# Kernel optimization log

Hardware: AMD Instinct MI355X
Metric: run time of the kernel (lower is better)

## Reference

```python
import jax, jax.numpy as jnp
import numpy as np

B, S, D, H = 2, 2048, 1024, 16
HD = D // H  # 64
MASK_VAL = -10000.0


def setup_inputs() -> dict:
    key = jax.random.key(0)
    ks = jax.random.split(key, 8)
    sc = 0.02
    q_features = jax.random.normal(ks[0], (B, S, D), jnp.float32)
    kv_features = jax.random.normal(ks[1], (B, S, D), jnp.float32)
    # causal mask, broadcastable (1,1,S,S)
    mask = jnp.tril(jnp.ones((S, S), jnp.bool_))[None, None]
    Wq = jax.random.normal(ks[2], (D, D), jnp.float32) * sc
    bq = jnp.zeros((D,), jnp.float32)
    Wkv = jax.random.normal(ks[3], (D, 2 * D), jnp.float32) * sc
    bkv = jnp.zeros((2 * D,), jnp.float32)
    Wp = jax.random.normal(ks[4], (D, D), jnp.float32) * sc
    bp = jnp.zeros((D,), jnp.float32)
    return {"q_features": q_features, "kv_features": kv_features, "mask": mask,
            "Wq": Wq, "bq": bq, "Wkv": Wkv, "bkv": bkv, "Wp": Wp, "bp": bp}


def _split_heads(t):
    # (B,S,D) -> (B,H,S,HD)
    return t.reshape(B, S, H, HD).transpose(0, 2, 1, 3)


def reference(q_features, kv_features, mask, Wq, bq, Wkv, bkv, Wp, bp):
    query = q_features @ Wq + bq            # (B,S,D)
    kv = kv_features @ Wkv + bkv            # (B,S,2D)
    key, value = jnp.split(kv, 2, axis=-1)
    q = _split_heads(query)                 # (B,H,S,HD)
    k = _split_heads(key)
    v = _split_heads(value)
    scores = jnp.einsum('bhqd,bhkd->bhqk', q, k) / jnp.sqrt(jnp.float32(HD))
    scores = jnp.where(mask, scores, jnp.asarray(MASK_VAL, scores.dtype))
    attn = jax.nn.softmax(scores, axis=-1)  # (B,H,S,S)
    out = jnp.einsum('bhqk,bhkd->bhqd', attn, v)
    out = out.transpose(0, 2, 1, 3).reshape(B, S, D)  # merge heads
    return out @ Wp + bp
```

## Files before the change

### kernel.cpp

```cpp
#include <hip/hip_runtime.h>

typedef unsigned short u16;
typedef unsigned int u32;
typedef __attribute__((ext_vector_type(4))) unsigned short us4;
typedef __attribute__((ext_vector_type(8))) unsigned short us8;
typedef __attribute__((ext_vector_type(4))) short s16x4;
typedef __attribute__((ext_vector_type(8))) __bf16 bf16x8;
typedef __attribute__((ext_vector_type(4))) float floatx4;

#define S_ 2048
#define D_ 1024
#define QSC 0.18033688f

__device__ __forceinline__ float b2f(u16 u) {
  unsigned v = ((unsigned)u) << 16;
  return __builtin_bit_cast(float, v);
}
__device__ __forceinline__ u16 f2bf(float f) {
  unsigned u = __builtin_bit_cast(unsigned, f);
  unsigned r = (u + 0x7fffu + ((u >> 16) & 1u)) >> 16;
  return (u16)r;
}
__device__ __forceinline__ u16 f2bf_rhu(float f) {
  return (u16)((__builtin_bit_cast(unsigned, f) + 0x8000u) >> 16);
}

typedef const __attribute__((address_space(1))) u32* gas_t;
typedef __attribute__((address_space(3))) u32* las_t;
__device__ __forceinline__ void gload16(const u16* g, u16* l) {
  __builtin_amdgcn_global_load_lds((gas_t)g, (las_t)l, 16, 0, 0);
}

#define PBAR()                                   \
  {                                              \
    __builtin_amdgcn_sched_barrier(0);           \
    asm volatile("" ::: "memory");               \
    __builtin_amdgcn_s_barrier();                \
    asm volatile("" ::: "memory");               \
    __builtin_amdgcn_sched_barrier(0);           \
  }
#define WAITVM(N) asm volatile("s_waitcnt vmcnt(" #N ")" ::: "memory")

__global__ __launch_bounds__(256) void prep(
    const float* __restrict__ qf, const float* __restrict__ kvf,
    const float* __restrict__ Wq, const float* __restrict__ Wkv,
    const float* __restrict__ Wp, u16* __restrict__ qa, u16* __restrict__ kva,
    u16* __restrict__ Wqt, u16* __restrict__ Wkvt, u16* __restrict__ Wpt) {
  int bid = blockIdx.x, tid = threadIdx.x;
  if (bid < 4096) {
    const float* src = (bid < 2048) ? qf : kvf;
    u16* dst = (bid < 2048) ? qa : kva;
    size_t i = ((size_t)(bid & 2047) * 256 + tid) * 8;
    floatx4 a = *(const floatx4*)(src + i);
    floatx4 b = *(const floatx4*)(src + i + 4);
    us8 r;
#pragma unroll
    for (int j = 0; j < 4; j++) { r[j] = f2bf(a[j]); r[4 + j] = f2bf(b[j]); }
    *(us8*)(dst + i) = r;
  } else {
    int t = bid - 4096;
    const float* src; u16* dst; int R, C;
    if (t < 1024)      { src = Wq;  dst = Wqt;  R = 1024; C = 1024; }
    else if (t < 3072) { t -= 1024; src = Wkv; dst = Wkvt; R = 1024; C = 2048; }
    else               { t -= 3072; src = Wp;  dst = Wpt;  R = 1024; C = 1024; }
    int bx = t % (C >> 5), by = t / (C >> 5);
    __shared__ u16 tile[32][33];
    int tx = tid & 31, ty = tid >> 5;
    int x = bx * 32 + tx;
    for (int i = ty; i < 32; i += 8)
      tile[i][tx] = f2bf(src[(size_t)(by * 32 + i) * C + x]);
    __syncthreads();
    int r = tid >> 3, c4 = tid & 7;
    us4 v;
#pragma unroll
    for (int j = 0; j < 4; j++) v[j] = tile[c4 * 4 + j][r];
    *(us4*)&dst[(size_t)(bx * 32 + r) * R + by * 32 + c4 * 4] = v;
  }
}

template <int MODE>
__device__ __forceinline__ void gemm256(
    const u16* __restrict__ A, const u16* __restrict__ Bt,
    const float* __restrict__ bias, void* __restrict__ C0,
    u16* __restrict__ C1, int N, int m0, int n0, u16* smem, float cscale) {
  int tid = threadIdx.x;
  int w = tid >> 6, lane = tid & 63;
  int quad = lane >> 4, l16 = lane & 15;
  int wr = w >> 2, wc = w & 3;

  int srow = w * 32 + (lane >> 2);
  int gchunk = ((lane & 3) ^ ((lane >> 3) & 3)) << 3;
  const u16* Asrc = A + (size_t)(m0 + srow) * 1024 + gchunk;
  const u16* Bsrc = Bt + (size_t)(n0 + srow) * 1024 + gchunk;
  u16* Adst = smem + w * 1024;
  u16* Bdst = smem + 32768 + w * 1024;

  int swz = (quad ^ ((l16 >> 1) & 3)) << 3;
  int aoff = (wr * 128 + l16) * 32 + swz;
  int boff = 32768 + (wc * 64 + l16) * 32 + swz;

  floatx4 acc[8][4] = {};

#define STG(t)                                                 \
  {                                                            \
    int s_ = (t) & 3;                                          \
    gload16(Asrc + (t) * 32, Adst + s_ * 8192);                \
    gload16(Asrc + (t) * 32 + 16384, Adst + s_ * 8192 + 512);  \
    gload16(Bsrc + (t) * 32, Bdst + s_ * 8192);                \
    gload16(Bsrc + (t) * 32 + 16384, Bdst + s_ * 8192 + 512);  \
  }

  STG(0); STG(1); STG(2);
  WAITVM(8);
  PBAR();

#pragma unroll 1
  for (int t = 0; t < 32; t++) {
    int so = (t & 3) * 8192;
    bf16x8 af[8], bf[4];
#pragma unroll
    for (int mf = 0; mf < 8; mf++)
      af[mf] = __builtin_bit_cast(bf16x8,
          *(const us8*)&smem[so + aoff + mf * 512]);
#pragma unroll
    for (int nf = 0; nf < 4; nf++)
      bf[nf] = __builtin_bit_cast(bf16x8,
          *(const us8*)&smem[so + boff + nf * 512]);
    if (t < 29) STG(t + 3);
    __builtin_amdgcn_s_setprio(1);
#pragma unroll
    for (int mf = 0; mf < 8; mf++)
#pragma unroll
      for (int nf = 0; nf < 4; nf++)
        acc[mf][nf] = __builtin_amdgcn_mfma_f32_16x16x32_bf16(
            af[mf], bf[nf], acc[mf][nf], 0, 0, 0);
    __builtin_amdgcn_s_setprio(0);
    if (t < 29)      { WAITVM(8); }
    else if (t == 29){ WAITVM(4); }
    else if (t == 30){ WAITVM(0); }
    if (t < 31) PBAR();
  }
#undef STG

#pragma unroll
  for (int mf = 0; mf < 8; mf++) {
#pragma unroll
    for (int nf = 0; nf < 4; nf++) {
      int col = n0 + wc * 64 + nf * 16 + l16;
      int rowq = m0 + wr * 128 + mf * 16 + quad * 4;
      float bv = bias[col];
      if (MODE == 0) {
        u16* o = (u16*)C0;
#pragma unroll
        for (int r = 0; r < 4; r++)
          o[(size_t)(rowq + r) * N + col] = f2bf((acc[mf][nf][r] + bv) * cscale);
      } else {
        if (col < 1024) {
          u16* o = (u16*)C0;
#pragma unroll
          for (int r = 0; r < 4; r++)
            o[(size_t)(rowq + r) * 1024 + col] = f2bf(acc[mf][nf][r] + bv);
        } else {
          int vcol = col - 1024;
          int b = rowq >> 11, s0 = rowq & 2047;
          us4 pv;
#pragma unroll
          for (int r = 0; r < 4; r++) pv[r] = f2bf(acc[mf][nf][r] + bv);
          *(us4*)&C1[((size_t)(b * 1024 + vcol)) * (size_t)S_ + s0] = pv;
        }
      }
    }
  }
}

__global__ __launch_bounds__(512, 2) void gemm_qkv(
    const u16* __restrict__ qa, const u16* __restrict__ kva,
    const u16* __restrict__ Wqt, const u16* __restrict__ Wkvt,
    const float* __restrict__ bq, const float* __restrict__ bkv,
    u16* __restrict__ Qb, u16* __restrict__ Kb, u16* __restrict__ Vt) {
  __shared__ __align__(16) u16 smem[65536];
  int bid = blockIdx.x;
  int work = (bid & 7) * 24 + (bid >> 3);
  if (work < 64) {
    gemm256<0>(qa, Wqt, bq, Qb, nullptr, 1024,
               (work >> 2) * 256, (work & 3) * 256, smem, QSC);
  } else {
    int lb = work - 64;
    gemm256<2>(kva, Wkvt, bkv, Kb, Vt, 2048,
               (lb >> 3) * 256, (lb & 7) * 256, smem, 1.0f);
  }
}

__device__ __forceinline__ void gemm_out_core(
    const u16* __restrict__ A, const u16* __restrict__ Bt,
    const float* __restrict__ bias, float* __restrict__ C,
    int m0, int n0, u16* smem) {
  int tid = threadIdx.x;
  int w = tid >> 6, lane = tid & 63;
  int quad = lane >> 4, l16 = lane & 15;
  int wr = w >> 1, wc = w & 1;

  int gchunk = ((lane & 3) ^ ((lane >> 3) & 3)) << 3;
  const u16* Ag = A + (size_t)(m0 + w * 32 + (lane >> 2)) * 1024 + gchunk;
  const u16* Bg = Bt + (size_t)(n0 + w * 16 + (lane >> 2)) * 1024 + gchunk;
  u16* Adst = smem + w * 1024;
  u16* Bdst = smem + 4096 + w * 512;

  int swz = (quad ^ ((l16 >> 1) & 3)) << 3;
  int aoff = (wr * 64 + l16) * 32 + swz;
  int boff = 4096 + (wc * 32 + l16) * 32 + swz;

  floatx4 acc[4][2] = {};

#define STGO(t)                                                \
  {                                                            \
    int s_ = (t) & 3;                                          \
    gload16(Ag + (t) * 32, Adst + s_ * 6144);                  \
    gload16(Ag + (t) * 32 + 16384, Adst + s_ * 6144 + 512);    \
    gload16(Bg + (t) * 32, Bdst + s_ * 6144);                  \
  }

  STGO(0); STGO(1); STGO(2);
  WAITVM(6);
  PBAR();

#pragma unroll 1
  for (int t = 0; t < 32; t++) {
    int so = (t & 3) * 6144;
    bf16x8 af[4], bf[2];
#pragma unroll
    for (int mf = 0; mf < 4; mf++)
      af[mf] = __builtin_bit_cast(bf16x8,
          *(const us8*)&smem[so + aoff + mf * 512]);
#pragma unroll
    for (int nf = 0; nf < 2; nf++)
      bf[nf] = __builtin_bit_cast(bf16x8,
          *(const us8*)&smem[so + boff + nf * 512]);
    if (t < 29) STGO(t + 3);
    __builtin_amdgcn_s_setprio(1);
#pragma unroll
    for (int mf = 0; mf < 4; mf++)
#pragma unroll
      for (int nf = 0; nf < 2; nf++)
        acc[mf][nf] = __builtin_amdgcn_mfma_f32_16x16x32_bf16(
            af[mf], bf[nf], acc[mf][nf], 0, 0, 0);
    __builtin_amdgcn_s_setprio(0);
    if (t < 29)      { WAITVM(6); }
    else if (t == 29){ WAITVM(3); }
    else if (t == 30){ WAITVM(0); }
    if (t < 31) PBAR();
  }
#undef STGO

#pragma unroll
  for (int mf = 0; mf < 4; mf++) {
#pragma unroll
    for (int nf = 0; nf < 2; nf++) {
      int col = n0 + wc * 32 + nf * 16 + l16;
      int rowq = m0 + wr * 64 + mf * 16 + quad * 4;
      float bv = bias[col];
#pragma unroll
      for (int r = 0; r < 4; r++)
        C[(size_t)(rowq + r) * 1024 + col] = acc[mf][nf][r] + bv;
    }
  }
}

__global__ __launch_bounds__(256, 2) void gemm_out(
    const u16* __restrict__ AO, const u16* __restrict__ Wpt,
    const float* __restrict__ bp, float* __restrict__ out) {
  __shared__ __align__(16) u16 smem[24576];
  int work = (blockIdx.x & 7) * 64 + (blockIdx.x >> 3);
  gemm_out_core(AO, Wpt, bp, out, (work >> 4) * 128, (work & 15) * 64, smem);
}

__global__ __launch_bounds__(512, 4) void attn_fwd(
    const u16* __restrict__ Q, const u16* __restrict__ Kb,
    const u16* __restrict__ Vt, u16* __restrict__ O,
    u16* __restrict__ Opart, float* __restrict__ ml) {
  __shared__ __align__(16) u16 sm[16384];
  int tid  = threadIdx.x;
  int w    = tid >> 6, lane = tid & 63;
  int quad = lane >> 4, l16 = lane & 15;
  int bh = blockIdx.x, b = bh >> 4, h = bh & 15;
  int y = blockIdx.y;

  static const signed char yt_[12] = {7,7,3,6,6,5,5,2,4,4,1,0};
  static const signed char yh_[12] = {0,1,-1,0,1,0,1,-1,0,1,-1,-1};
  int t = yt_[y], hh = yh_[y];
  bool split = hh >= 0;
  int kb0, kb1;
  if (split) { kb0 = hh ? (2 * t + 2) : 0; kb1 = hh ? (4 * t + 4) : (2 * t + 2); }
  else       { kb0 = 0; kb1 = 4 * t + 4; }
  int n = kb1 - kb0;

  const size_t row0 = (size_t)b * S_;
  const u16* Kg = Kb + row0 * D_ + h * 64;
  const u16* Vg = Vt + ((size_t)b * 1024 + h * 64) * S_;

  int qlo = t * 256 + w * 32;
  int dkb = qlo >> 6;
  int qgb = (w & 1) * 32;

  const u16* qp = Q + (row0 + qlo + l16) * D_ + h * 64 + quad * 8;
  bf16x8 aq[2][2];
  aq[0][0] = __builtin_bit_cast(bf16x8, *(const us8*)(qp));
  aq[0][1] = __builtin_bit_cast(bf16x8, *(const us8*)(qp + 32));
  aq[1][0] = __builtin_bit_cast(bf16x8, *(const us8*)(qp + (size_t)16 * D_));
  aq[1][1] = __builtin_bit_cast(bf16x8, *(const us8*)(qp + (size_t)16 * D_ + 32));

  floatx4 o_[2][4] = {};
  floatx4 l_acc[2] = {};
  const s16x4 ones4 = {0x3F80, 0x3F80, 0x3F80, 0x3F80};

  int srow = tid >> 3, c8 = tid & 7;
  int woff = srow * 64 + ((c8 ^ (srow & 7)) << 3);
  u16* smK = sm;
  u16* smV = sm + 8192;

  const u16* Kp = Kg + (size_t)(kb0 * 64 + srow) * D_ + c8 * 8;
  const u16* Vp = Vg + (size_t)srow * S_ + kb0 * 64 + c8 * 8;
  us8 pk = *(const us8*)Kp, pv = *(const us8*)Vp;
  *(us8*)&smK[woff] = pk;
  *(us8*)&smV[woff] = pv;
  if (n > 1) {
    Kp += (size_t)64 * D_; Vp += 64;
    pk = *(const us8*)Kp; pv = *(const us8*)Vp;
  }
  __syncthreads();

  for (int i = 0; i < n; i++) {
    int cur = i & 1;
    int kb = kb0 + i;
    if (i + 1 < n) {
      int nxt = (cur ^ 1) * 4096;
      *(us8*)&smK[nxt + woff] = pk;
      *(us8*)&smV[nxt + woff] = pv;
      if (i + 2 < n) {
        Kp += (size_t)64 * D_; Vp += 64;
        pk = *(const us8*)Kp; pv = *(const us8*)Vp;
      }
    }
    if (kb <= dkb) {
      const u16* Ksb = smK + cur * 4096;
      const u16* Vsb = smV + cur * 4096;

      floatx4 s[2][4] = {};
      __builtin_amdgcn_s_setprio(1);
#pragma unroll
      for (int kk = 0; kk < 2; kk++)
#pragma unroll
        for (int nt = 0; nt < 4; nt++) {
          us8 kf = *(const us8*)&Ksb[(nt * 16 + l16) * 64 +
                                     (((kk * 4 + quad) ^ (l16 & 7)) << 3)];
          bf16x8 kfb = __builtin_bit_cast(bf16x8, kf);
          s[0][nt] = __builtin_amdgcn_mfma_f32_16x16x32_bf16(
              kfb, aq[0][kk], s[0][nt], 0, 0, 0);
          s[1][nt] = __builtin_amdgcn_mfma_f32_16x16x32_bf16(
              kfb, aq[1][kk], s[1][nt], 0, 0, 0);
        }
      __builtin_amdgcn_s_setprio(0);

      if (kb == dkb) {
#pragma unroll
        for (int hf = 0; hf < 2; hf++) {
          int qg = qgb + hf * 16 + l16;
#pragma unroll
          for (int nt = 0; nt < 4; nt++)
#pragma unroll
            for (int r = 0; r < 4; r++)
              if (nt * 16 + quad * 4 + r > qg) s[hf][nt][r] = -1e5f;
        }
      }

      s16x4 pb[2][4];
#pragma unroll
      for (int hf = 0; hf < 2; hf++)
#pragma unroll
        for (int nt = 0; nt < 4; nt++)
#pragma unroll
          for (int r = 0; r < 4; r++)
            pb[hf][nt][r] = (short)f2bf_rhu(__builtin_amdgcn_exp2f(s[hf][nt][r]));

      __builtin_amdgcn_s_setprio(1);
#pragma unroll
      for (int nt = 0; nt < 4; nt++) {
        l_acc[0] = __builtin_amdgcn_mfma_f32_16x16x16bf16_1k(ones4, pb[0][nt], l_acc[0], 0, 0, 0);
        l_acc[1] = __builtin_amdgcn_mfma_f32_16x16x16bf16_1k(ones4, pb[1][nt], l_acc[1], 0, 0, 0);
#pragma unroll
        for (int mt = 0; mt < 4; mt++) {
          int hd = mt * 16 + l16;
          int chunk = nt * 2 + (quad >> 1);
          us4 vf = *(const us4*)&Vsb[hd * 64 + ((chunk ^ (l16 & 7)) << 3) + (quad & 1) * 4];
          s16x4 vb = __builtin_bit_cast(s16x4, vf);
          o_[0][mt] = __builtin_amdgcn_mfma_f32_16x16x16bf16_1k(
              vb, pb[0][nt], o_[0][mt], 0, 0, 0);
          o_[1][mt] = __builtin_amdgcn_mfma_f32_16x16x16bf16_1k(
              vb, pb[1][nt], o_[1][mt], 0, 0, 0);
        }
      }
      __builtin_amdgcn_s_setprio(0);
    }
    __syncthreads();
  }

  if (!split) {
#pragma unroll
    for (int hf = 0; hf < 2; hf++) {
      float rl = __builtin_amdgcn_rcpf(l_acc[hf][0]);
      size_t orow = (row0 + qlo + hf * 16 + l16) * D_ + h * 64;
#pragma unroll
      for (int mt = 0; mt < 4; mt++) {
        us4 ov;
#pragma unroll
        for (int r = 0; r < 4; r++) ov[r] = f2bf(o_[hf][mt][r] * rl);
        *(us4*)&O[orow + mt * 16 + quad * 4] = ov;
      }
    }
  } else {
    int part = (t - 4) * 2 + hh;
    u16* op = Opart + ((size_t)(bh * 8 + part)) * 16384;
#pragma unroll
    for (int hf = 0; hf < 2; hf++) {
      int rloc = w * 32 + hf * 16 + l16;
#pragma unroll
      for (int mt = 0; mt < 4; mt++) {
        us4 ov;
#pragma unroll
        for (int r = 0; r < 4; r++) ov[r] = f2bf(o_[hf][mt][r]);
        *(us4*)&op[rloc * 64 + mt * 16 + quad * 4] = ov;
      }
      if (quad == 0)
        ml[(size_t)(bh * 8 + part) * 256 + rloc] = l_acc[hf][0];
    }
  }
}

__global__ __launch_bounds__(256) void combine(
    const u16* __restrict__ Opart, const float* __restrict__ ml,
    u16* __restrict__ O) {
  int bh = blockIdx.x, b = bh >> 4, h = bh & 15;
  int t = 4 + blockIdx.y;
  int p0 = bh * 8 + (t - 4) * 2;
  const u16* o1 = Opart + (size_t)p0 * 16384;
  const u16* o2 = o1 + 16384;
  int row = threadIdx.x;
  float l1 = ml[(size_t)p0 * 256 + row];
  float l2 = ml[(size_t)(p0 + 1) * 256 + row];
  float inv = __builtin_amdgcn_rcpf(l1 + l2);
  size_t orow = ((size_t)b * S_ + t * 256 + row) * D_ + h * 64;
#pragma unroll
  for (int v = 0; v < 8; v++) {
    us8 x1 = *(const us8*)&o1[row * 64 + v * 8];
    us8 x2 = *(const us8*)&o2[row * 64 + v * 8];
    us8 out;
#pragma unroll
    for (int j = 0; j < 8; j++)
      out[j] = f2bf((b2f(x1[j]) + b2f(x2[j])) * inv);
    *(us8*)&O[orow + v * 8] = out;
  }
}

extern "C" void kernel_launch(void* const* d_in, const int* in_sizes, int n_in,
                              void* d_out, int out_size, void* d_ws, size_t ws_size,
                              hipStream_t stream) {
  const float* qf  = (const float*)d_in[0];
  const float* kvf = (const float*)d_in[1];
  const float* Wq  = (const float*)d_in[3];
  const float* bq  = (const float*)d_in[4];
  const float* Wkv = (const float*)d_in[5];
  const float* bkv = (const float*)d_in[6];
  const float* Wp  = (const float*)d_in[7];
  const float* bp  = (const float*)d_in[8];

  char* ws = (char*)d_ws;
  const size_t MB = 1048576;
  u16*   kva  = (u16*)(ws);
  u16*   AO   = (u16*)(ws);
  u16*   Kbp  = (u16*)(ws + 8 * MB);
  u16*   Vtp  = (u16*)(ws + 16 * MB);
  u16*   Wqt  = (u16*)(ws + 24 * MB);
  float* mlp  = (float*)(ws + 24 * MB);
  u16*   Wkvt = (u16*)(ws + 26 * MB);
  u16*   Wpt  = (u16*)(ws + 30 * MB);
  u16*   qa    = (u16*)d_out;
  u16*   Opart = (u16*)d_out;
  u16*   Qb    = (u16*)d_out + (size_t)4 * 1048576;

  prep<<<8192, 256, 0, stream>>>(qf, kvf, Wq, Wkv, Wp, qa, kva, Wqt, Wkvt, Wpt);
  gemm_qkv<<<192, 512, 0, stream>>>(qa, kva, Wqt, Wkvt, bq, bkv, Qb, Kbp, Vtp);
  attn_fwd<<<dim3(32, 12), 512, 0, stream>>>(Qb, Kbp, Vtp, AO, Opart, mlp);
  combine<<<dim3(32, 4), 256, 0, stream>>>(Opart, mlp, AO);
  gemm_out<<<512, 256, 0, stream>>>(AO, Wpt, bp, (float*)d_out);
}
```

Baseline: 208.4 us.

## Software-pipeline attention: overlap QK^T of block i with PV of block i-1

Restructures the attention inner loop so each iteration issues the QK^T MFMAs for the current key block, then the PV MFMAs for the previous block, then the mask and exp2 for the current scores. This lets the exp/convert work overlap with matrix ops. LDS grows from double to triple buffering (indexed modulo 3) so the previous V block stays valid, and an epilogue drains the last PV step. The cost is higher register pressure from carrying probabilities across iterations, and more shared memory, which may reduce occupancy.

```diff
diff --git a/kernel.cpp b/kernel.cpp
--- a/kernel.cpp
+++ b/kernel.cpp
@@ -278,7 +278,7 @@
     const u16* __restrict__ Q, const u16* __restrict__ Kb,
     const u16* __restrict__ Vt, u16* __restrict__ O,
     u16* __restrict__ Opart, float* __restrict__ ml) {
-  __shared__ __align__(16) u16 sm[16384];
+  __shared__ __align__(16) u16 sm[24576];
   int tid  = threadIdx.x;
   int w    = tid >> 6, lane = tid & 63;
   int quad = lane >> 4, l16 = lane & 15;
@@ -316,36 +316,42 @@
   int srow = tid >> 3, c8 = tid & 7;
   int woff = srow * 64 + ((c8 ^ (srow & 7)) << 3);
   u16* smK = sm;
-  u16* smV = sm + 8192;
+  u16* smV = sm + 12288;
 
   const u16* Kp = Kg + (size_t)(kb0 * 64 + srow) * D_ + c8 * 8;
   const u16* Vp = Vg + (size_t)srow * S_ + kb0 * 64 + c8 * 8;
   us8 pk = *(const us8*)Kp, pv = *(const us8*)Vp;
-  *(us8*)&smK[woff] = pk;
-  *(us8*)&smV[woff] = pv;
+  {
+    int sl0 = kb0 % 3;
+    *(us8*)&smK[sl0 * 4096 + woff] = pk;
+    *(us8*)&smV[sl0 * 4096 + woff] = pv;
+  }
   if (n > 1) {
     Kp += (size_t)64 * D_; Vp += 64;
     pk = *(const us8*)Kp; pv = *(const us8*)Vp;
   }
   __syncthreads();
 
-  for (int i = 0; i < n; i++) {
-    int cur = i & 1;
-    int kb = kb0 + i;
-    if (i + 1 < n) {
-      int nxt = (cur ^ 1) * 4096;
-      *(us8*)&smK[nxt + woff] = pk;
-      *(us8*)&smV[nxt + woff] = pv;
-      if (i + 2 < n) {
+  s16x4 pbp[2][4];
+  bool prevAct = false;
+  int prevSlot = 0;
+
+  for (int i = kb0; i < kb1; i++) {
+    int slot = i % 3;
+    if (i + 1 < kb1) {
+      int ws = (i + 1) % 3;
+      *(us8*)&smK[ws * 4096 + woff] = pk;
+      *(us8*)&smV[ws * 4096 + woff] = pv;
+      if (i + 2 < kb1) {
         Kp += (size_t)64 * D_; Vp += 64;
         pk = *(const us8*)Kp; pv = *(const us8*)Vp;
       }
     }
-    if (kb <= dkb) {
-      const u16* Ksb = smK + cur * 4096;
-      const u16* Vsb = smV + cur * 4096;
-
-      floatx4 s[2][4] = {};
+    bool act = (i <= dkb);
+    floatx4 s[2][4] = {};
+
+    if (act) {
+      const u16* Ksb = smK + slot * 4096;
       __builtin_amdgcn_s_setprio(1);
 #pragma unroll
       for (int kk = 0; kk < 2; kk++)
@@ -360,33 +366,15 @@
               kfb, aq[1][kk], s[1][nt], 0, 0, 0);
         }
       __builtin_amdgcn_s_setprio(0);
-
-      if (kb == dkb) {
-#pragma unroll
-        for (int hf = 0; hf < 2; hf++) {
-          int qg = qgb + hf * 16 + l16;
-#pragma unroll
-          for (int nt = 0; nt < 4; nt++)
-#pragma unroll
-            for (int r = 0; r < 4; r++)
-              if (nt * 16 + quad * 4 + r > qg) s[hf][nt][r] = -1e5f;
-        }
-      }
-
-      s16x4 pb[2][4];
-#pragma unroll
-      for (int hf = 0; hf < 2; hf++)
-#pragma unroll
-        for (int nt = 0; nt < 4; nt++)
-#pragma unroll
-          for (int r = 0; r < 4; r++)
-            pb[hf][nt][r] = (short)f2bf_rhu(__builtin_amdgcn_exp2f(s[hf][nt][r]));
-
+    }
+
+    if (prevAct) {
+      const u16* Vsb = smV + prevSlot * 4096;
       __builtin_amdgcn_s_setprio(1);
 #pragma unroll
       for (int nt = 0; nt < 4; nt++) {
-        l_acc[0] = __builtin_amdgcn_mfma_f32_16x16x16bf16_1k(ones4, pb[0][nt], l_acc[0], 0, 0, 0);
-        l_acc[1] = __builtin_amdgcn_mfma_f32_16x16x16bf16_1k(ones4, pb[1][nt], l_acc[1], 0, 0, 0);
+        l_acc[0] = __builtin_amdgcn_mfma_f32_16x16x16bf16_1k(ones4, pbp[0][nt], l_acc[0], 0, 0, 0);
+        l_acc[1] = __builtin_amdgcn_mfma_f32_16x16x16bf16_1k(ones4, pbp[1][nt], l_acc[1], 0, 0, 0);
 #pragma unroll
         for (int mt = 0; mt < 4; mt++) {
           int hd = mt * 16 + l16;
@@ -394,14 +382,57 @@
           us4 vf = *(const us4*)&Vsb[hd * 64 + ((chunk ^ (l16 & 7)) << 3) + (quad & 1) * 4];
           s16x4 vb = __builtin_bit_cast(s16x4, vf);
           o_[0][mt] = __builtin_amdgcn_mfma_f32_16x16x16bf16_1k(
-              vb, pb[0][nt], o_[0][mt], 0, 0, 0);
+              vb, pbp[0][nt], o_[0][mt], 0, 0, 0);
           o_[1][mt] = __builtin_amdgcn_mfma_f32_16x16x16bf16_1k(
-              vb, pb[1][nt], o_[1][mt], 0, 0, 0);
+              vb, pbp[1][nt], o_[1][mt], 0, 0, 0);
         }
       }
       __builtin_amdgcn_s_setprio(0);
     }
+
+    if (act) {
+      if (i == dkb) {
+#pragma unroll
+        for (int hf = 0; hf < 2; hf++) {
+          int qg = qgb + hf * 16 + l16;
+#pragma unroll
+          for (int nt = 0; nt < 4; nt++)
+#pragma unroll
+            for (int r = 0; r < 4; r++)
+              if (nt * 16 + quad * 4 + r > qg) s[hf][nt][r] = -1e5f;
+        }
+      }
+#pragma unroll
+      for (int hf = 0; hf < 2; hf++)
+#pragma unroll
+        for (int nt = 0; nt < 4; nt++)
+#pragma unroll
+          for (int r = 0; r < 4; r++)
+            pbp[hf][nt][r] = (short)f2bf_rhu(__builtin_amdgcn_exp2f(s[hf][nt][r]));
+    }
+    prevAct = act;
+    prevSlot = slot;
     __syncthreads();
+  }
+
+  if (prevAct) {
+    const u16* Vsb = smV + prevSlot * 4096;
+#pragma unroll
+    for (int nt = 0; nt < 4; nt++) {
+      l_acc[0] = __builtin_amdgcn_mfma_f32_16x16x16bf16_1k(ones4, pbp[0][nt], l_acc[0], 0, 0, 0);
+      l_acc[1] = __builtin_amdgcn_mfma_f32_16x16x16bf16_1k(ones4, pbp[1][nt], l_acc[1], 0, 0, 0);
+#pragma unroll
+      for (int mt = 0; mt < 4; mt++) {
+        int hd = mt * 16 + l16;
+        int chunk = nt * 2 + (quad >> 1);
+        us4 vf = *(const us4*)&Vsb[hd * 64 + ((chunk ^ (l16 & 7)) << 3) + (quad & 1) * 4];
+        s16x4 vb = __builtin_bit_cast(s16x4, vf);
+        o_[0][mt] = __builtin_amdgcn_mfma_f32_16x16x16bf16_1k(
+            vb, pbp[0][nt], o_[0][mt], 0, 0, 0);
+        o_[1][mt] = __builtin_amdgcn_mfma_f32_16x16x16bf16_1k(
+            vb, pbp[1][nt], o_[1][mt], 0, 0, 0);
+      }
+    }
   }
 
   if (!split) {
```

After: 239.7 us. 15.0% more time.
